# Kernel optimization log

Measured on AMD Instinct MI355X. Metric: run time of the kernel, lower is better.

The kernel has to match this reference:

```python
import jax, jax.numpy as jnp
import numpy as np

# dims
N, T, F, DEMO, H, NHEAD, K, GCN, FFN = 4096, 48, 76, 4, 252, 4, 10, 256, 128
D = H + DEMO          # 256, input dim to graph constructor / clustering / gcn
DK = D // NHEAD       # 64
TAU, MASK_P, LAMBDA_KL, LAMBDA_CL, PHI_INIT, ALPHA = 0.5, 0.1, 1.0, 1.0, 3.0 / N, 1.0


def setup_inputs() -> dict:
    key = jax.random.key(0)
    ks = jax.random.split(key, 16)
    s = 0.02
    return dict(
        x=jax.random.normal(ks[0], (N, T, F), jnp.float32),
        x_demo=jax.random.normal(ks[1], (N, DEMO), jnp.float32),
        sorted_length=jax.random.randint(ks[2], (N,), 1, T + 1),
        mask_edge=jax.random.uniform(ks[3], (N, N), jnp.float32),
        w_ih=jax.random.normal(ks[4], (3 * H, F), jnp.float32) * s,
        w_hh=jax.random.normal(ks[5], (3 * H, H), jnp.float32) * s,
        b_ih=jnp.zeros((3 * H,), jnp.float32),
        b_hh=jnp.zeros((3 * H,), jnp.float32),
        h0=jnp.zeros((H,), jnp.float32),
        wq=jax.random.normal(ks[6], (D, D), jnp.float32) * s,
        bq=jnp.zeros((D,), jnp.float32),
        wk=jax.random.normal(ks[7], (D, D), jnp.float32) * s,
        bk=jnp.zeros((D,), jnp.float32),
        wo=jax.random.normal(ks[8], (NHEAD,), jnp.float32) * s,
        bo=jnp.zeros((), jnp.float32),
        phi=jnp.float32(PHI_INIT),
        centers=jax.random.normal(ks[9], (K, D), jnp.float32),
        gcn_w=jax.random.normal(ks[10], (D, GCN), jnp.float32) * s,
        gcn_b=jnp.zeros((GCN,), jnp.float32),
        ffn_w=jax.random.normal(ks[11], (GCN, FFN), jnp.float32) * s,
        ffn_b=jnp.zeros((FFN,), jnp.float32),
        pre_w=jax.random.normal(ks[12], (GCN, 2), jnp.float32) * s,
        pre_b=jnp.zeros((2,), jnp.float32),
    )


def _forward(x, x_demo, sorted_length, mask_edge, w_ih, w_hh, b_ih, b_hh, h0,
             wq, bq, wk, bk, wo, bo, phi, centers, gcn_w, gcn_b,
             ffn_w, ffn_b, pre_w, pre_b):
    n = x.shape[0]

    # --- GRU over time (torch nn.GRU equations), scan over T ---
    def gru_step(h, xt):
        gi = xt @ w_ih.T + b_ih                     # [N, 3H]
        gh = h @ w_hh.T + b_hh
        ir, iz, inn = jnp.split(gi, 3, axis=-1)
        hr, hz, hn = jnp.split(gh, 3, axis=-1)
        r = jax.nn.sigmoid(ir + hr)
        zg = jax.nn.sigmoid(iz + hz)
        ng = jnp.tanh(inn + r * hn)
        h = (1.0 - zg) * ng + zg * h
        return h, h

    _, outs = jax.lax.scan(gru_step, jnp.broadcast_to(h0, (n, H)), jnp.swapaxes(x, 0, 1))
    idx = jnp.clip(sorted_length - 1, 0, T - 1)
    x_gru = outs[idx, jnp.arange(n)]                # last valid hidden state [N, H]
    x_star = jnp.concatenate([x_gru, x_demo], axis=1)  # [N, D]

    # --- GraphConstructor: multi-head attention adjacency ---
    q = (x_star @ wq.T + bq).reshape(n, NHEAD, DK)
    kk = (x_star @ wk.T + bk).reshape(n, NHEAD, DK)
    scores = jnp.einsum('nhd,mhd->nmh', q, kk) / np.sqrt(DK)  # [N, N, h]
    scores = scores @ wo + bo                                  # Wo: Linear(h, 1)
    attn = jax.nn.softmax(scores, axis=1)
    eye = jnp.eye(n, dtype=x.dtype)
    adj = jnp.where(attn >= phi, 1.0, 0.0) * (1.0 - eye)       # threshold, zero diag

    # --- Clustering: soft assignment around given centers (KMeans fit replaced
    #     by fixed cluster_layer parameter; same soft-assign / KLD math) ---
    d2 = jnp.sum((x_star[:, None, :] - centers[None]) ** 2, axis=-1)  # [N, K]
    qsoft = 1.0 / (1.0 + d2 / ALPHA)
    qsoft = qsoft / jnp.sum(qsoft, axis=1, keepdims=True)
    pdist = qsoft ** 2 / jnp.sum(qsoft, axis=0, keepdims=True)
    pdist = jax.lax.stop_gradient(pdist / jnp.sum(pdist, axis=1, keepdims=True))
    label = jnp.argmax(qsoft, axis=1)
    kl_loss = jnp.mean(jnp.sum(pdist * jnp.log(pdist / (qsoft + 1e-6)), axis=-1))

    # --- GCNConv on dense adjacency (sym-normalized with self loops) ---
    xw = x_star @ gcn_w

    def gcn(a):
        a_hat = a + eye
        dinv = 1.0 / jnp.sqrt(jnp.sum(a_hat, axis=1))
        return (dinv[:, None] * a_hat * dinv[None, :]) @ xw + gcn_b

    z = gcn(adj)
    adj_aug = adj * (mask_edge >= MASK_P).astype(x.dtype)  # DataAug edge mask (bernoulli keep 1-p)
    z_aug = gcn(adj_aug)
    zf = z @ ffn_w + ffn_b
    zfa = z_aug @ ffn_w + ffn_b

    # --- clloss: NxN contrastive loss ---
    def l2n(a):
        return a / jnp.clip(jnp.linalg.norm(a, axis=1, keepdims=True), 1e-12, None)

    zn, zan = l2n(zf), l2n(zfa)
    intra = jnp.exp(zn @ zn.T / TAU)
    inter = jnp.exp(zn @ zan.T / TAU)
    cadj = (label[:, None] == label[None, :]).astype(x.dtype) * (1.0 - eye)
    cadj_new = jnp.where(adj == 1.0, 0.0, cadj)
    positive = jnp.diag(inter) + jnp.sum(intra * adj, axis=1) + jnp.sum(intra * cadj_new, axis=1)
    denom = jnp.sum(intra, axis=1) + jnp.sum(inter, axis=1) - jnp.diag(intra)
    cnt = jnp.sum(adj, axis=1) + jnp.sum(cadj_new, axis=1) + 1.0
    cl_loss = -jnp.sum(jnp.log(positive / denom) / cnt)

    loss = LAMBDA_KL * kl_loss + LAMBDA_CL * cl_loss
    output = z @ pre_w + pre_b
    return output, loss


def reference(x, x_demo, sorted_length, mask_edge, w_ih, w_hh, b_ih, b_hh, h0,
              wq, bq, wk, bk, wo, bo, phi, centers, gcn_w, gcn_b,
              ffn_w, ffn_b, pre_w, pre_b):
    return _forward(x, x_demo, sorted_length, mask_edge, w_ih, w_hh, b_ih, b_hh, h0,
                    wq, bq, wk, bk, wo, bo, phi, centers, gcn_w, gcn_b,
                    ffn_w, ffn_b, pre_w, pre_b)
```

## Files before the change

kernel.cpp:

```cpp
#include <hip/hip_runtime.h>
#include <cstdint>
#include <cstddef>

typedef _Float16 f16;
typedef f16 f16x8 __attribute__((ext_vector_type(8)));
typedef float f32x4 __attribute__((ext_vector_type(4)));

#define MFMA(a,b,c) __builtin_amdgcn_mfma_f32_16x16x32_f16(a,b,c,0,0,0)

__device__ __forceinline__ float sigm(float x){ return 1.f/(1.f+__expf(-x)); }
__device__ __forceinline__ float tanh_f(float x){
  float a = __expf(-2.f*fabsf(x));
  float t = (1.f-a)/(1.f+a);
  return x >= 0.f ? t : -t;
}
__device__ __forceinline__ uint16_t f2bf(float f){
  uint32_t u = __float_as_uint(f);
  return (uint16_t)((u + 0x7fffu + ((u>>16)&1u)) >> 16);
}
__device__ __forceinline__ float bf2f(uint16_t h){
  return __uint_as_float(((uint32_t)h) << 16);
}

__global__ __launch_bounds__(256) void k_prep(
    const float* __restrict__ w_ih, const float* __restrict__ w_hh,
    const float* __restrict__ b_ih, const float* __restrict__ b_hh,
    const int* __restrict__ slen,
    const float* __restrict__ wq, const float* __restrict__ wk,
    const float* __restrict__ gcn_w,
    f16* __restrict__ BgT, f16* __restrict__ wq16, f16* __restrict__ wk16,
    f16* __restrict__ gw16, float* __restrict__ biasc, int* __restrict__ idx)
{
  int id = blockIdx.x*256 + threadIdx.x;
  if (id < 360448){
    int g = id / (256*352); int rem = id % (256*352);
    int j = rem / 352; int k = rem % 352;
    float v = 0.f;
    if (j < 252){
      if (k < 96){
        if (k < 76 && g != 3){
          int row = (g==2) ? (504+j) : (g*252+j);
          v = w_ih[row*76 + k];
        }
      } else {
        int kh = k - 96;
        if (kh < 252 && g != 2){
          int row = (g==3) ? (504+j) : (g*252+j);
          v = w_hh[row*252 + kh];
        }
      }
    }
    BgT[id] = (f16)v;
    return;
  }
  id -= 360448;
  if (id < 65536){ wq16[id] = (f16)wq[id]; return; }
  id -= 65536;
  if (id < 65536){ wk16[id] = (f16)wk[id]; return; }
  id -= 65536;
  if (id < 65536){ int j = id >> 8, d = id & 255; gw16[id] = (f16)gcn_w[d*256 + j]; return; }
  id -= 65536;
  if (id < 1008){
    int g = id / 252, j = id % 252; float v;
    if (g==0) v = b_ih[j] + b_hh[j];
    else if (g==1) v = b_ih[252+j] + b_hh[252+j];
    else if (g==2) v = b_ih[504+j];
    else v = b_hh[504+j];
    biasc[id] = v; return;
  }
  id -= 1008;
  if (id < 4096){
    int s = slen[id] - 1; s = s < 0 ? 0 : (s > 47 ? 47 : s);
    idx[id] = s; return;
  }
}

__global__ __launch_bounds__(256) void k_xt(const float* __restrict__ x,
    f16* __restrict__ x16t)
{
  int id = blockIdx.x*256 + threadIdx.x;
  int c = id % 12; int rem = id / 12;
  int n = rem & 4095; int t = rem >> 12;
  const float* xp = x + ((size_t)n*48 + t)*76;
  f16x8 o;
  #pragma unroll
  for (int e = 0; e < 8; ++e){
    int k = c*8 + e;
    o[e] = (k < 76) ? (f16)xp[k] : (f16)0.f;
  }
  *(f16x8*)(x16t + ((size_t)t*4096 + n)*96 + c*8) = o;
}

__global__ __launch_bounds__(1024, 4) void k_gru_all(
    const f16* __restrict__ x16t, const f16* __restrict__ BgT,
    const float* __restrict__ biasc, const float* __restrict__ h0,
    const int* __restrict__ idxp, float* __restrict__ xstar,
    f16* __restrict__ xs16)
{
  __shared__ f16 hbuf[2][32][256];
  __shared__ f16 wc[7][16][512];
  __shared__ int idxl[32];
  int lane = threadIdx.x & 63, w = threadIdx.x >> 6;
  int l16 = lane & 15, lq = lane >> 4;
  int nb = blockIdx.x * 32;

  for (int i = threadIdx.x; i < 32*256; i += 1024){
    int row = i >> 8, c = i & 255;
    int sc = (((c >> 3) ^ (row & 7)) << 3) | (c & 7);
    hbuf[0][row][sc] = (c < 252) ? (f16)h0[c] : (f16)0.f;
  }
  if (threadIdx.x < 32) idxl[threadIdx.x] = idxp[nb + threadIdx.x];

  int j = w*16 + l16;
  bool jv = (j < 252);
  int js = jv ? j : 251;
  float bR = biasc[js], bZ = biasc[252+js], bI = biasc[504+js], bH = biasc[756+js];
  const f16* pR = BgT + (size_t)(0*256 + j)*352 + lq*8;
  const f16* pZ = BgT + (size_t)(1*256 + j)*352 + lq*8;
  const f16* pI = BgT + (size_t)(2*256 + j)*352 + lq*8;
  const f16* pH = BgT + (size_t)(3*256 + j)*352 + lq*8;
  const f16* xp0 = x16t + ((size_t)nb + l16)*96 + lq*8;
  const f16* xp1 = x16t + ((size_t)nb + 16 + l16)*96 + lq*8;

  *(f16x8*)&wc[0][w][lane*8] = *(const f16x8*)(pR);
  *(f16x8*)&wc[1][w][lane*8] = *(const f16x8*)(pZ);
  *(f16x8*)&wc[2][w][lane*8] = *(const f16x8*)(pI);
  *(f16x8*)&wc[3][w][lane*8] = *(const f16x8*)(pR + 32);
  *(f16x8*)&wc[4][w][lane*8] = *(const f16x8*)(pZ + 32);
  *(f16x8*)&wc[5][w][lane*8] = *(const f16x8*)(pI + 32);
  *(f16x8*)&wc[6][w][lane*8] = *(const f16x8*)(pR + 64);

  float hown[2][4];
  #pragma unroll
  for (int mf = 0; mf < 2; ++mf)
  #pragma unroll
  for (int r = 0; r < 4; ++r)
    hown[mf][r] = jv ? h0[js] : 0.f;

  __syncthreads();

  for (int t = 0; t < 48; ++t){
    const f16 (*hin)[256] = hbuf[t & 1];
    f16 (*hout)[256]      = hbuf[(t & 1) ^ 1];
    f32x4 z4 = {0.f,0.f,0.f,0.f};
    f32x4 aR[2] = {z4,z4}, aZ[2] = {z4,z4}, aI[2] = {z4,z4}, aH[2] = {z4,z4};
    size_t xt = (size_t)t*4096*96;

    f16x8 R0,Z0,M0, R1,Z1,M1, R2,Z2,M2, R3,Z3,M3;
#define PIN3(s) asm volatile("" :: "v"(*(const f32x4*)&R##s), \
                                   "v"(*(const f32x4*)&Z##s), \
                                   "v"(*(const f32x4*)&M##s))
#define PIN2(s) asm volatile("" :: "v"(*(const f32x4*)&Z##s), \
                                   "v"(*(const f32x4*)&M##s))
#define LW(s,u) do{ \
      R##s = *(const f16x8*)(pR + (u)*32); \
      Z##s = *(const f16x8*)(pZ + (u)*32); \
      M##s = *(const f16x8*)((((u) < 3) ? pI : pH) + (u)*32); \
      PIN3(s); }while(0)
#define LW2(s,u) do{ \
      Z##s = *(const f16x8*)(pZ + (u)*32); \
      M##s = *(const f16x8*)((((u) < 3) ? pI : pH) + (u)*32); \
      PIN2(s); }while(0)
#define MM(u, wR_, wZ_, wM_, a0, a1) do{ \
      aR[0] = MFMA(a0, wR_, aR[0]);  aR[1] = MFMA(a1, wR_, aR[1]); \
      aZ[0] = MFMA(a0, wZ_, aZ[0]);  aZ[1] = MFMA(a1, wZ_, aZ[1]); \
      if ((u) < 3){ aI[0] = MFMA(a0, wM_, aI[0]);  aI[1] = MFMA(a1, wM_, aI[1]); } \
      else        { aH[0] = MFMA(a0, wM_, aH[0]);  aH[1] = MFMA(a1, wM_, aH[1]); } \
    }while(0)
#define STEP(s,u) do{ \
      f16x8 a0, a1; \
      if ((u) < 3){ \
        a0 = *(const f16x8*)(xp0 + xt + (u)*32); \
        a1 = *(const f16x8*)(xp1 + xt + (u)*32); \
      } else { \
        int chunk = ((u) - 3)*4 + lq; \
        a0 = *(const f16x8*)(&hin[l16][(chunk ^ (l16 & 7)) << 3]); \
        a1 = *(const f16x8*)(&hin[16 + l16][(chunk ^ (l16 & 7)) << 3]); \
      } \
      MM(u, R##s, Z##s, M##s, a0, a1); \
    }while(0)
#define STEP_L(u) do{ \
      f16x8 wR_ = *(const f16x8*)&wc[(u)*3+0][w][lane*8]; \
      f16x8 wZ_ = *(const f16x8*)&wc[(u)*3+1][w][lane*8]; \
      f16x8 wM_ = *(const f16x8*)&wc[(u)*3+2][w][lane*8]; \
      f16x8 a0 = *(const f16x8*)(xp0 + xt + (u)*32); \
      f16x8 a1 = *(const f16x8*)(xp1 + xt + (u)*32); \
      MM(u, wR_, wZ_, wM_, a0, a1); \
    }while(0)
#define STEP2(s,u) do{ \
      f16x8 wR_ = *(const f16x8*)&wc[6][w][lane*8]; \
      f16x8 a0 = *(const f16x8*)(xp0 + xt + (u)*32); \
      f16x8 a1 = *(const f16x8*)(xp1 + xt + (u)*32); \
      MM(u, wR_, Z##s, M##s, a0, a1); \
    }while(0)

    LW2(0,2); LW(1,3); LW(2,4); LW(3,5);
    STEP_L(0);
    STEP_L(1);
    STEP2(0,2);  LW(0,6);
    STEP(1,3);   LW(1,7);
    STEP(2,4);   LW(2,8);
    STEP(3,5);   LW(3,9);
    STEP(0,6);   LW(0,10);
    STEP(1,7);
    STEP(2,8);
    STEP(3,9);
    STEP(0,10);
#undef LW
#undef LW2
#undef STEP
#undef STEP_L
#undef STEP2
#undef MM
#undef PIN3
#undef PIN2

    #pragma unroll
    for (int mf = 0; mf < 2; ++mf)
    #pragma unroll
    for (int r = 0; r < 4; ++r){
      int row = mf*16 + lq*4 + r;
      float rr = sigm(aR[mf][r] + bR);
      float zz = sigm(aZ[mf][r] + bZ);
      float ng = tanh_f(aI[mf][r] + bI + rr*(aH[mf][r] + bH));
      float hnew = (1.f - zz)*ng + zz*hown[mf][r];
      hnew = jv ? hnew : 0.f;
      hown[mf][r] = hnew;
      int sc = (((j >> 3) ^ (row & 7)) << 3) | (j & 7);
      hout[row][sc] = (f16)hnew;
      if (jv && idxl[row] == t){
        xstar[((size_t)(nb + row) << 8) + j] = hnew;
        xs16[((size_t)(nb + row) << 8) + j] = (f16)hnew;
      }
    }
    __syncthreads();
  }
}

__global__ __launch_bounds__(256) void k_xdemo(const float* __restrict__ x_demo,
    float* __restrict__ xs32, f16* __restrict__ xs16)
{
  int id = blockIdx.x*256 + threadIdx.x;
  int n = id >> 2, c = id & 3;
  float v = x_demo[id];
  xs32[((size_t)n << 8) + 252 + c] = v;
  xs16[((size_t)n << 8) + 252 + c] = (f16)v;
}

template<int MODE>
__global__ __launch_bounds__(256) void k_proj(const f16* __restrict__ xs16,
    const f16* __restrict__ w16, const float* __restrict__ bias,
    const float* __restrict__ wo, f16* __restrict__ out16)
{
  int lane = threadIdx.x & 63, wv = threadIdx.x >> 6;
  int l16 = lane & 15, lq = lane >> 4;
  int nb = blockIdx.x * 64;
  int ocol = blockIdx.y*64 + wv*16 + l16;
  f32x4 z4 = {0.f,0.f,0.f,0.f};
  f32x4 acc[4] = {z4,z4,z4,z4};
  #pragma unroll
  for (int ks = 0; ks < 8; ++ks){
    f16x8 b = *(const f16x8*)(w16 + (size_t)ocol*256 + ks*32 + lq*8);
    #pragma unroll
    for (int mi = 0; mi < 4; ++mi){
      f16x8 a = *(const f16x8*)(xs16 + (size_t)(nb + mi*16 + l16)*256 + ks*32 + lq*8);
      acc[mi] = MFMA(a, b, acc[mi]);
    }
  }
  float badd = bias[ocol];
  float scale = (MODE == 0) ? wo[ocol >> 6]*0.125f : 1.f;
  #pragma unroll
  for (int mi = 0; mi < 4; ++mi)
  #pragma unroll
  for (int r = 0; r < 4; ++r){
    int n = nb + mi*16 + lq*4 + r;
    float v = acc[mi][r] + badd;
    if (MODE == 0) v *= scale;
    out16[(size_t)n*256 + ocol] = (f16)v;
  }
}

__global__ __launch_bounds__(256) void k_scores(const f16* __restrict__ qf,
    const f16* __restrict__ kf, uint16_t* __restrict__ sco)
{
  int lane = threadIdx.x & 63, w = threadIdx.x >> 6;
  int l16 = lane & 15, lq = lane >> 4;
  int mh = w >> 1, jh = w & 1;
  int nb = blockIdx.x*128 + mh*64;
  int mb = blockIdx.y*128 + jh*64;
  f32x4 z4 = {0.f,0.f,0.f,0.f};
  f32x4 acc[4][4];
  #pragma unroll
  for (int i = 0; i < 4; ++i)
  #pragma unroll
  for (int j = 0; j < 4; ++j) acc[i][j] = z4;
  #pragma unroll
  for (int ks = 0; ks < 8; ++ks){
    f16x8 a[4], b[4];
    #pragma unroll
    for (int i = 0; i < 4; ++i){
      a[i] = *(const f16x8*)(qf + (size_t)(nb + i*16 + l16)*256 + ks*32 + lq*8);
      b[i] = *(const f16x8*)(kf + (size_t)(mb + i*16 + l16)*256 + ks*32 + lq*8);
    }
    #pragma unroll
    for (int mi = 0; mi < 4; ++mi)
    #pragma unroll
    for (int jf = 0; jf < 4; ++jf)
      acc[mi][jf] = MFMA(a[mi], b[jf], acc[mi][jf]);
  }
  #pragma unroll
  for (int mi = 0; mi < 4; ++mi)
  #pragma unroll
  for (int jf = 0; jf < 4; ++jf)
  #pragma unroll
  for (int r = 0; r < 4; ++r){
    int n = nb + mi*16 + lq*4 + r;
    int m = mb + jf*16 + l16;
    sco[((size_t)n << 12) + m] = f2bf(acc[mi][jf][r]);
  }
}

__global__ __launch_bounds__(256) void k_adj(const uint16_t* __restrict__ sco,
    const float* __restrict__ mask_edge, const float* __restrict__ phip,
    uint8_t* __restrict__ flags, float* __restrict__ sadj,
    float* __restrict__ dinv, float* __restrict__ dinva)
{
  int n = blockIdx.x;
  int lane = threadIdx.x & 63, wv = threadIdx.x >> 6;
  const uint16_t* row = sco + ((size_t)n << 12);
  int base = threadIdx.x * 16;
  const uint4* p = (const uint4*)(row + base);
  uint4 w0 = p[0], w1 = p[1];
  uint32_t ws_[8] = {w0.x,w0.y,w0.z,w0.w,w1.x,w1.y,w1.z,w1.w};
  float v[16];
  #pragma unroll
  for (int i = 0; i < 8; ++i){
    v[2*i]   = bf2f((uint16_t)(ws_[i] & 0xffffu));
    v[2*i+1] = bf2f((uint16_t)(ws_[i] >> 16));
  }
  float mx = v[0];
  #pragma unroll
  for (int i = 1; i < 16; ++i) mx = fmaxf(mx, v[i]);
  #pragma unroll
  for (int o = 32; o >= 1; o >>= 1) mx = fmaxf(mx, __shfl_xor(mx, o));
  __shared__ float redA[4], redB[4], redC[4], redD[4];
  if (lane == 0) redA[wv] = mx;
  __syncthreads();
  mx = fmaxf(fmaxf(redA[0], redA[1]), fmaxf(redA[2], redA[3]));
  float s = 0.f;
  #pragma unroll
  for (int i = 0; i < 16; ++i){ v[i] = __expf(v[i] - mx); s += v[i]; }
  #pragma unroll
  for (int o = 32; o >= 1; o >>= 1) s += __shfl_xor(s, o);
  if (lane == 0) redB[wv] = s;
  __syncthreads();
  float rs = 1.f / (redB[0] + redB[1] + redB[2] + redB[3]);
  float phi = phip[0];
  uint32_t by[16]; int c0 = 0, c1 = 0;
  #pragma unroll
  for (int e = 0; e < 16; ++e){
    float a = v[e] * rs;
    int col = base + e;
    uint32_t b = (a >= phi && col != n) ? 1u : 0u;
    if (b){ if (mask_edge[((size_t)n << 12) + col] >= 0.1f) b |= 2u; }
    by[e] = b;
    c0 += (int)(b & 1u);
    c1 += (int)(b >> 1);
  }
  uint4 pk;
  pk.x = by[0]  | (by[1]  << 8) | (by[2]  << 16) | (by[3]  << 24);
  pk.y = by[4]  | (by[5]  << 8) | (by[6]  << 16) | (by[7]  << 24);
  pk.z = by[8]  | (by[9]  << 8) | (by[10] << 16) | (by[11] << 24);
  pk.w = by[12] | (by[13] << 8) | (by[14] << 16) | (by[15] << 24);
  *(uint4*)(flags + ((size_t)n << 12) + base) = pk;
  float f0 = (float)c0, f1 = (float)c1;
  #pragma unroll
  for (int o = 32; o >= 1; o >>= 1){ f0 += __shfl_xor(f0, o); f1 += __shfl_xor(f1, o); }
  if (lane == 0){ redC[wv] = f0; redD[wv] = f1; }
  __syncthreads();
  if (threadIdx.x == 0){
    float d0 = redC[0]+redC[1]+redC[2]+redC[3];
    float d1 = redD[0]+redD[1]+redD[2]+redD[3];
    sadj[n] = d0;
    dinv[n]  = rsqrtf(1.f + d0);
    dinva[n] = rsqrtf(1.f + d1);
  }
}

__global__ __launch_bounds__(256) void k_xw_y(const f16* __restrict__ xs16,
    const f16* __restrict__ gw16, const float* __restrict__ dinv,
    const float* __restrict__ dinva, f16* __restrict__ y16, f16* __restrict__ ya16)
{
  int lane = threadIdx.x & 63, wv = threadIdx.x >> 6;
  int l16 = lane & 15, lq = lane >> 4;
  int nb = blockIdx.x * 64;
  int jcol = blockIdx.y*64 + wv*16 + l16;
  f32x4 z4 = {0.f,0.f,0.f,0.f};
  f32x4 acc[4] = {z4,z4,z4,z4};
  #pragma unroll
  for (int ks = 0; ks < 8; ++ks){
    f16x8 b = *(const f16x8*)(gw16 + (size_t)jcol*256 + ks*32 + lq*8);
    #pragma unroll
    for (int mi = 0; mi < 4; ++mi){
      f16x8 a = *(const f16x8*)(xs16 + (size_t)(nb + mi*16 + l16)*256 + ks*32 + lq*8);
      acc[mi] = MFMA(a, b, acc[mi]);
    }
  }
  #pragma unroll
  for (int mi = 0; mi < 4; ++mi)
  #pragma unroll
  for (int r = 0; r < 4; ++r){
    int n = nb + mi*16 + lq*4 + r;
    float v = acc[mi][r];
    y16[(size_t)n*256 + jcol]  = (f16)(dinv[n]*v);
    ya16[(size_t)n*256 + jcol] = (f16)(dinva[n]*v);
  }
}

__global__ __launch_bounds__(256) void k_zgather(const uint8_t* __restrict__ flags,
    const f16* __restrict__ y16, const f16* __restrict__ ya16,
    const float* __restrict__ dinv, const float* __restrict__ dinva,
    const float* __restrict__ gcn_b, float* __restrict__ z32, float* __restrict__ za32)
{
  int n = blockIdx.x;
  int lane = threadIdx.x & 63, wv = threadIdx.x >> 6;
  uint4 w = ((const uint4*)(flags + ((size_t)n << 12)))[threadIdx.x];
  uint32_t m0[4] = {w.x & 0x01010101u, w.y & 0x01010101u, w.z & 0x01010101u, w.w & 0x01010101u};
  uint32_t m1[4] = {w.x & 0x02020202u, w.y & 0x02020202u, w.z & 0x02020202u, w.w & 0x02020202u};
  int c0 = __popc(m0[0]) + __popc(m0[1]) + __popc(m0[2]) + __popc(m0[3]);
  int c1 = __popc(m1[0]) + __popc(m1[1]) + __popc(m1[2]) + __popc(m1[3]);
  int v0 = c0, v1 = c1;
  #pragma unroll
  for (int o = 1; o < 64; o <<= 1){
    int u0 = __shfl_up(v0, o), u1 = __shfl_up(v1, o);
    if (lane >= o){ v0 += u0; v1 += u1; }
  }
  __shared__ int wsum0[4], wsum1[4];
  if (lane == 63){ wsum0[wv] = v0; wsum1[wv] = v1; }
  __syncthreads();
  int pos0 = v0 - c0, pos1 = v1 - c1;
  #pragma unroll
  for (int i = 0; i < 4; ++i) if (i < wv){ pos0 += wsum0[i]; pos1 += wsum1[i]; }
  int tot0 = wsum0[0]+wsum0[1]+wsum0[2]+wsum0[3];
  int tot1 = wsum1[0]+wsum1[1]+wsum1[2]+wsum1[3];
  __shared__ uint16_t list0[4096];
  __shared__ uint16_t list1[4096];
  int cbase = threadIdx.x * 16;
  #pragma unroll
  for (int q = 0; q < 4; ++q){
    uint32_t m = m0[q];
    while (m){
      int b = __ffs(m) - 1;
      list0[pos0++] = (uint16_t)(cbase + q*4 + (b >> 3));
      m &= m - 1;
    }
    m = m1[q];
    while (m){
      int b = __ffs(m) - 1;
      list1[pos1++] = (uint16_t)(cbase + q*4 + (b >> 3));
      m &= m - 1;
    }
  }
  __syncthreads();
  int j = threadIdx.x;
  float acc0 = (float)y16[((size_t)n << 8) + j];
  float acc1 = (float)ya16[((size_t)n << 8) + j];
  for (int i = 0; i < tot0; ++i) acc0 += (float)y16[((size_t)list0[i] << 8) + j];
  for (int i = 0; i < tot1; ++i) acc1 += (float)ya16[((size_t)list1[i] << 8) + j];
  z32[((size_t)n << 8) + j]  = dinv[n]*acc0 + gcn_b[j];
  za32[((size_t)n << 8) + j] = dinva[n]*acc1 + gcn_b[j];
}

__global__ __launch_bounds__(256) void k_cluster(const float* __restrict__ xs32,
    const float* __restrict__ centers, float* __restrict__ qsoft,
    int* __restrict__ labels, float* __restrict__ colsum)
{
  int nb = blockIdx.x * 16;
  __shared__ float xs[16][256];
  __shared__ float ct[2560];
  __shared__ float d2s[16][10];
  __shared__ float qs[16][10];
  for (int i = threadIdx.x; i < 16*256; i += 256) xs[i >> 8][i & 255] = xs32[(size_t)nb*256 + i];
  for (int i = threadIdx.x; i < 2560; i += 256){ int k = i >> 8, d = i & 255; ct[d*10 + k] = centers[i]; }
  __syncthreads();
  if (threadIdx.x < 160){
    int r = threadIdx.x / 10, k = threadIdx.x % 10;
    float s = 0.f;
    for (int d = 0; d < 256; ++d){ float df = xs[r][d] - ct[d*10 + k]; s += df*df; }
    d2s[r][k] = s;
  }
  __syncthreads();
  if (threadIdx.x < 16){
    int r = threadIdx.x;
    float un[10]; float tot = 0.f;
    #pragma unroll
    for (int k = 0; k < 10; ++k){ un[k] = 1.f/(1.f + d2s[r][k]); tot += un[k]; }
    float inv = 1.f / tot;
    int best = 0; float bm = un[0];
    #pragma unroll
    for (int k = 1; k < 10; ++k){ if (un[k] > bm){ bm = un[k]; best = k; } }
    labels[nb + r] = best;
    #pragma unroll
    for (int k = 0; k < 10; ++k){ float q = un[k]*inv; qs[r][k] = q; qsoft[(size_t)(nb + r)*10 + k] = q; }
  }
  __syncthreads();
  if (threadIdx.x < 10){
    int k = threadIdx.x; float s = 0.f;
    #pragma unroll
    for (int r = 0; r < 16; ++r) s += qs[r][k];
    atomicAdd(&colsum[k], s);
  }
}

__global__ __launch_bounds__(256) void k_kl(const float* __restrict__ qsoft,
    const float* __restrict__ colsum, float* __restrict__ klsum)
{
  int n = blockIdx.x*256 + threadIdx.x;
  float p[10]; float s = 0.f;
  #pragma unroll
  for (int k = 0; k < 10; ++k){
    float q = qsoft[(size_t)n*10 + k];
    float pu = q*q/colsum[k];
    p[k] = pu; s += pu;
  }
  float inv = 1.f/s; float kl = 0.f;
  #pragma unroll
  for (int k = 0; k < 10; ++k){
    float pk = p[k]*inv;
    float q = qsoft[(size_t)n*10 + k];
    kl += pk*__logf(pk/(q + 1e-6f));
  }
  int lane = threadIdx.x & 63, wv = threadIdx.x >> 6;
  #pragma unroll
  for (int o = 32; o >= 1; o >>= 1) kl += __shfl_xor(kl, o);
  __shared__ float red[4];
  if (lane == 0) red[wv] = kl;
  __syncthreads();
  if (threadIdx.x == 0) atomicAdd(klsum, red[0]+red[1]+red[2]+red[3]);
}

__global__ __launch_bounds__(128) void k_ffn(const float* __restrict__ z32,
    const float* __restrict__ za32, const float* __restrict__ ffn_w,
    const float* __restrict__ ffn_b, f16* __restrict__ zn16, f16* __restrict__ zan16)
{
  int n = blockIdx.x; int aug = blockIdx.y;
  const float* z = (aug ? za32 : z32) + ((size_t)n << 8);
  __shared__ float zr[256];
  zr[threadIdx.x] = z[threadIdx.x];
  zr[threadIdx.x + 128] = z[threadIdx.x + 128];
  __syncthreads();
  int j = threadIdx.x;
  float acc = ffn_b[j];
  #pragma unroll 8
  for (int d = 0; d < 256; ++d) acc += zr[d]*ffn_w[d*128 + j];
  float ss = acc*acc;
  int lane = threadIdx.x & 63, wv = threadIdx.x >> 6;
  #pragma unroll
  for (int o = 32; o >= 1; o >>= 1) ss += __shfl_xor(ss, o);
  __shared__ float sred[2];
  if (lane == 0) sred[wv] = ss;
  __syncthreads();
  float tot = sred[0] + sred[1];
  float rn = 1.f / fmaxf(sqrtf(tot), 1e-12f);
  (aug ? zan16 : zn16)[((size_t)n << 7) + j] = (f16)(acc*rn);
}

__global__ __launch_bounds__(256) void k_closs(const f16* __restrict__ zn,
    const f16* __restrict__ zan, const uint8_t* __restrict__ flags,
    const int* __restrict__ labels,
    float* __restrict__ rs1, float* __restrict__ rs2, float* __restrict__ rsA,
    float* __restrict__ rsC, float* __restrict__ rcC, float* __restrict__ rdI,
    float* __restrict__ rdi)
{
  int lane = threadIdx.x & 63;
  int ji = threadIdx.x >> 6;
  int l16 = lane & 15, lq = lane >> 4;
  int nb = blockIdx.x * 32;
  int mstart = blockIdx.y * 512;
  f16x8 A[2][4];
  #pragma unroll
  for (int mi = 0; mi < 2; ++mi)
  #pragma unroll
  for (int ks = 0; ks < 4; ++ks)
    A[mi][ks] = *(const f16x8*)(zn + (size_t)(nb + mi*16 + l16)*128 + ks*32 + lq*8);
  int labn[8];
  #pragma unroll
  for (int i = 0; i < 8; ++i) labn[i] = labels[nb + (i >> 2)*16 + lq*4 + (i & 3)];
  float a1[8]={}, a2[8]={}, aA[8]={}, aC[8]={}, aCc[8]={}, adI[8]={}, adi[8]={};
  uint8_t fA[8]; int labA;
  {
    int mcol0 = mstart + ji*16 + l16;
    #pragma unroll
    for (int i = 0; i < 8; ++i){
      int n = nb + (i >> 2)*16 + lq*4 + (i & 3);
      fA[i] = flags[((size_t)n << 12) + mcol0];
    }
    labA = labels[mcol0];
  }
  #pragma unroll
  for (int tile = 0; tile < 8; ++tile){
    int mcol = mstart + tile*64 + ji*16 + l16;
    uint8_t fB[8]; int labB = 0;
    if (tile < 7){
      int mn = mcol + 64;
      #pragma unroll
      for (int i = 0; i < 8; ++i){
        int n = nb + (i >> 2)*16 + lq*4 + (i & 3);
        fB[i] = flags[((size_t)n << 12) + mn];
      }
      labB = labels[mn];
    }
    f32x4 z4 = {0.f,0.f,0.f,0.f};
    f32x4 acc1[2] = {z4, z4};
    f32x4 acc2[2] = {z4, z4};
    #pragma unroll
    for (int ks = 0; ks < 4; ++ks){
      f16x8 b1 = *(const f16x8*)(zn  + (size_t)mcol*128 + ks*32 + lq*8);
      f16x8 b2 = *(const f16x8*)(zan + (size_t)mcol*128 + ks*32 + lq*8);
      #pragma unroll
      for (int mi = 0; mi < 2; ++mi){
        acc1[mi] = MFMA(A[mi][ks], b1, acc1[mi]);
        acc2[mi] = MFMA(A[mi][ks], b2, acc2[mi]);
      }
    }
    #pragma unroll
    for (int mi = 0; mi < 2; ++mi)
    #pragma unroll
    for (int r = 0; r < 4; ++r){
      int i8 = mi*4 + r;
      int n = nb + mi*16 + lq*4 + r;
      float e1 = __expf(2.f*acc1[mi][r]);
      float e2 = __expf(2.f*acc2[mi][r]);
      uint8_t fl = fA[i8];
      a1[i8] += e1; a2[i8] += e2;
      bool adjb = (fl & 1);
      if (adjb) aA[i8] += e1;
      if (!adjb && labn[i8] == labA && n != mcol){ aC[i8] += e1; aCc[i8] += 1.f; }
      if (n == mcol){ adI[i8] += e2; adi[i8] += e1; }
    }
    if (tile < 7){
      #pragma unroll
      for (int i = 0; i < 8; ++i) fA[i] = fB[i];
      labA = labB;
    }
  }
  #pragma unroll
  for (int i = 0; i < 8; ++i){
    #pragma unroll
    for (int o = 1; o < 16; o <<= 1){
      a1[i]  += __shfl_xor(a1[i], o);  a2[i]  += __shfl_xor(a2[i], o);
      aA[i]  += __shfl_xor(aA[i], o);  aC[i]  += __shfl_xor(aC[i], o);
      aCc[i] += __shfl_xor(aCc[i], o); adI[i] += __shfl_xor(adI[i], o);
      adi[i] += __shfl_xor(adi[i], o);
    }
  }
  if (l16 == 0){
    #pragma unroll
    for (int i = 0; i < 8; ++i){
      int n = nb + (i >> 2)*16 + lq*4 + (i & 3);
      atomicAdd(&rs1[n], a1[i]);  atomicAdd(&rs2[n], a2[i]);
      atomicAdd(&rsA[n], aA[i]);  atomicAdd(&rsC[n], aC[i]);
      atomicAdd(&rcC[n], aCc[i]); atomicAdd(&rdI[n], adI[i]);
      atomicAdd(&rdi[n], adi[i]);
    }
  }
}

__global__ __launch_bounds__(256) void k_clfinal(const float* __restrict__ rs1,
    const float* __restrict__ rs2, const float* __restrict__ rsA,
    const float* __restrict__ rsC, const float* __restrict__ rcC,
    const float* __restrict__ rdI, const float* __restrict__ rdi,
    const float* __restrict__ sadj, float* __restrict__ clsum)
{
  int n = blockIdx.x*256 + threadIdx.x;
  float pos = rdI[n] + rsA[n] + rsC[n];
  float den = rs1[n] + rs2[n] - rdi[n];
  float cnt = sadj[n] + rcC[n] + 1.f;
  float v = __logf(pos/den)/cnt;
  int lane = threadIdx.x & 63, wv = threadIdx.x >> 6;
  #pragma unroll
  for (int o = 32; o >= 1; o >>= 1) v += __shfl_xor(v, o);
  __shared__ float red[4];
  if (lane == 0) red[wv] = v;
  __syncthreads();
  if (threadIdx.x == 0) atomicAdd(clsum, red[0]+red[1]+red[2]+red[3]);
}

__global__ void k_loss(const float* __restrict__ scal, float* __restrict__ out){
  out[8192] = scal[0]*(1.f/4096.f) - scal[1];
}

__global__ __launch_bounds__(256) void k_outhead(const float* __restrict__ z32,
    const float* __restrict__ pre_w, const float* __restrict__ pre_b,
    float* __restrict__ out)
{
  int lane = threadIdx.x & 63, wv = threadIdx.x >> 6;
  int n = blockIdx.x*4 + wv;
  float4 zv = *(const float4*)(z32 + ((size_t)n << 8) + lane*4);
  float4 w0 = *(const float4*)(pre_w + lane*8);
  float4 w1 = *(const float4*)(pre_w + lane*8 + 4);
  float c0 = zv.x*w0.x + zv.y*w0.z + zv.z*w1.x + zv.w*w1.z;
  float c1 = zv.x*w0.y + zv.y*w0.w + zv.z*w1.y + zv.w*w1.w;
  #pragma unroll
  for (int o = 32; o >= 1; o >>= 1){ c0 += __shfl_xor(c0, o); c1 += __shfl_xor(c1, o); }
  if (lane == 0){
    out[(size_t)n*2]     = c0 + pre_b[0];
    out[(size_t)n*2 + 1] = c1 + pre_b[1];
  }
}

extern "C" void kernel_launch(void* const* d_in, const int* in_sizes, int n_in,
                              void* d_out, int out_size, void* d_ws, size_t ws_size,
                              hipStream_t stream)
{
  const float* x         = (const float*)d_in[0];
  const float* x_demo    = (const float*)d_in[1];
  const int*   slen      = (const int*)d_in[2];
  const float* mask_edge = (const float*)d_in[3];
  const float* w_ih      = (const float*)d_in[4];
  const float* w_hh      = (const float*)d_in[5];
  const float* b_ih      = (const float*)d_in[6];
  const float* b_hh      = (const float*)d_in[7];
  const float* h0        = (const float*)d_in[8];
  const float* wq        = (const float*)d_in[9];
  const float* bq        = (const float*)d_in[10];
  const float* wk        = (const float*)d_in[11];
  const float* bk        = (const float*)d_in[12];
  const float* wo        = (const float*)d_in[13];
  const float* phi       = (const float*)d_in[15];
  const float* centers   = (const float*)d_in[16];
  const float* gcn_w     = (const float*)d_in[17];
  const float* gcn_b     = (const float*)d_in[18];
  const float* ffn_w     = (const float*)d_in[19];
  const float* ffn_b     = (const float*)d_in[20];
  const float* pre_w     = (const float*)d_in[21];
  const float* pre_b     = (const float*)d_in[22];
  float* out = (float*)d_out;

  size_t off = 0;
  char* base = (char*)d_ws;
  auto take = [&](size_t bytes)->void*{
    void* p = base + off;
    off += (bytes + 255) & ~(size_t)255;
    return p;
  };
  f16*   BgT    = (f16*)take((size_t)4*256*352*2);
  f16*   wq16   = (f16*)take((size_t)65536*2);
  f16*   wk16   = (f16*)take((size_t)65536*2);
  f16*   gw16   = (f16*)take((size_t)65536*2);
  float* biasc  = (float*)take(1008*4);
  int*   idx    = (int*)take(4096*4);
  float* xs32   = (float*)take((size_t)4096*256*4);
  f16*   xs16   = (f16*)take((size_t)4096*256*2);
  f16*   qf16   = (f16*)take((size_t)4096*256*2);
  f16*   kf16   = (f16*)take((size_t)4096*256*2);
  uint16_t* sco = (uint16_t*)take((size_t)4096*4096*2);
  uint8_t* flags= (uint8_t*)take((size_t)4096*4096);
  float* sadj   = (float*)take(4096*4);
  float* dinv   = (float*)take(4096*4);
  float* dinva  = (float*)take(4096*4);
  f16*   y16    = (f16*)take((size_t)4096*256*2);
  f16*   ya16   = (f16*)take((size_t)4096*256*2);
  float* z32    = (float*)take((size_t)4096*256*4);
  float* za32   = (float*)take((size_t)4096*256*4);
  f16*   zn16   = (f16*)take((size_t)4096*128*2);
  f16*   zan16  = (f16*)take((size_t)4096*128*2);
  float* qsoft  = (float*)take((size_t)4096*10*4);
  int*   labels = (int*)take(4096*4);
  float* colsum = (float*)take(64);
  float* scal   = (float*)take(64);
  float* rsbuf  = (float*)take((size_t)7*4096*4);
  float* rs1 = rsbuf,        *rs2 = rsbuf + 4096, *rsA = rsbuf + 2*4096;
  float* rsC = rsbuf + 3*4096, *rcC = rsbuf + 4*4096;
  float* rdI = rsbuf + 5*4096, *rdi = rsbuf + 6*4096;

  f16* x16t = (f16*)sco;

  hipMemsetAsync(colsum, 0, 64, stream);
  hipMemsetAsync(scal, 0, 64, stream);
  hipMemsetAsync(rsbuf, 0, (size_t)7*4096*4, stream);

  k_prep<<<2196, 256, 0, stream>>>(w_ih, w_hh, b_ih, b_hh, slen, wq, wk, gcn_w,
                                   BgT, wq16, wk16, gw16, biasc, idx);
  k_xt<<<9216, 256, 0, stream>>>(x, x16t);
  k_xdemo<<<64, 256, 0, stream>>>(x_demo, xs32, xs16);
  k_gru_all<<<128, 1024, 0, stream>>>(x16t, BgT, biasc, h0, idx, xs32, xs16);
  k_proj<0><<<dim3(64, 4), 256, 0, stream>>>(xs16, wq16, bq, wo, qf16);
  k_proj<1><<<dim3(64, 4), 256, 0, stream>>>(xs16, wk16, bk, wo, kf16);
  k_scores<<<dim3(32, 32), 256, 0, stream>>>(qf16, kf16, sco);
  k_adj<<<4096, 256, 0, stream>>>(sco, mask_edge, phi, flags, sadj, dinv, dinva);
  k_xw_y<<<dim3(64, 4), 256, 0, stream>>>(xs16, gw16, dinv, dinva, y16, ya16);
  k_zgather<<<4096, 256, 0, stream>>>(flags, y16, ya16, dinv, dinva, gcn_b, z32, za32);
  k_cluster<<<256, 256, 0, stream>>>(xs32, centers, qsoft, labels, colsum);
  k_kl<<<16, 256, 0, stream>>>(qsoft, colsum, &scal[0]);
  k_ffn<<<dim3(4096, 2), 128, 0, stream>>>(z32, za32, ffn_w, ffn_b, zn16, zan16);
  k_closs<<<dim3(128, 8), 256, 0, stream>>>(zn16, zan16, flags, labels,
                                            rs1, rs2, rsA, rsC, rcC, rdI, rdi);
  k_clfinal<<<16, 256, 0, stream>>>(rs1, rs2, rsA, rsC, rcC, rdI, rdi, sadj, &scal[1]);
  k_loss<<<1, 1, 0, stream>>>(scal, out);
  k_outhead<<<1024, 256, 0, stream>>>(z32, pre_w, pre_b, out);

  (void)in_sizes; (void)n_in; (void)out_size; (void)ws_size;
}
```

Measured before the change: 801.0 us.

## Single-buffer GRU hidden state, cache more weights in LDS, merge Q/K projections

The GRU kernel drops the double-buffered hidden-state array for one buffer with an extra barrier per step. It caches one more weight fragment (Z for the third chunk) in LDS, keeps the per-row output indices in registers instead of shared memory, and uses nontemporal loads for the streamed weights. The two Q/K projection launches become one kernel with a doubled grid. The extra barrier adds per-step sync cost in the serial recurrence, while the LDS and register savings and the dropped launch reduce overhead.

```diff
diff --git a/kernel.cpp b/kernel.cpp
--- a/kernel.cpp
+++ b/kernel.cpp
@@ -97,9 +97,8 @@
     const int* __restrict__ idxp, float* __restrict__ xstar,
     f16* __restrict__ xs16)
 {
-  __shared__ f16 hbuf[2][32][256];
-  __shared__ f16 wc[7][16][512];
-  __shared__ int idxl[32];
+  __shared__ f16 hbuf[32][256];
+  __shared__ f16 wc[8][16][512];
   int lane = threadIdx.x & 63, w = threadIdx.x >> 6;
   int l16 = lane & 15, lq = lane >> 4;
   int nb = blockIdx.x * 32;
@@ -107,9 +106,8 @@
   for (int i = threadIdx.x; i < 32*256; i += 1024){
     int row = i >> 8, c = i & 255;
     int sc = (((c >> 3) ^ (row & 7)) << 3) | (c & 7);
-    hbuf[0][row][sc] = (c < 252) ? (f16)h0[c] : (f16)0.f;
-  }
-  if (threadIdx.x < 32) idxl[threadIdx.x] = idxp[nb + threadIdx.x];
+    hbuf[row][sc] = (c < 252) ? (f16)h0[c] : (f16)0.f;
+  }
 
   int j = w*16 + l16;
   bool jv = (j < 252);
@@ -129,19 +127,23 @@
   *(f16x8*)&wc[4][w][lane*8] = *(const f16x8*)(pZ + 32);
   *(f16x8*)&wc[5][w][lane*8] = *(const f16x8*)(pI + 32);
   *(f16x8*)&wc[6][w][lane*8] = *(const f16x8*)(pR + 64);
+  *(f16x8*)&wc[7][w][lane*8] = *(const f16x8*)(pZ + 64);
 
   float hown[2][4];
+  int idxr[2][4];
   #pragma unroll
   for (int mf = 0; mf < 2; ++mf)
   #pragma unroll
-  for (int r = 0; r < 4; ++r)
+  for (int r = 0; r < 4; ++r){
     hown[mf][r] = jv ? h0[js] : 0.f;
-
-  __syncthreads();
+    idxr[mf][r] = idxp[nb + mf*16 + lq*4 + r];
+  }
+
+  __syncthreads();
+
+#define NTL(p) __builtin_nontemporal_load((const f16x8*)(p))
 
   for (int t = 0; t < 48; ++t){
-    const f16 (*hin)[256] = hbuf[t & 1];
-    f16 (*hout)[256]      = hbuf[(t & 1) ^ 1];
     f32x4 z4 = {0.f,0.f,0.f,0.f};
     f32x4 aR[2] = {z4,z4}, aZ[2] = {z4,z4}, aI[2] = {z4,z4}, aH[2] = {z4,z4};
     size_t xt = (size_t)t*4096*96;
@@ -150,17 +152,15 @@
 #define PIN3(s) asm volatile("" :: "v"(*(const f32x4*)&R##s), \
                                    "v"(*(const f32x4*)&Z##s), \
                                    "v"(*(const f32x4*)&M##s))
-#define PIN2(s) asm volatile("" :: "v"(*(const f32x4*)&Z##s), \
-                                   "v"(*(const f32x4*)&M##s))
+#define PIN1(s) asm volatile("" :: "v"(*(const f32x4*)&M##s))
 #define LW(s,u) do{ \
-      R##s = *(const f16x8*)(pR + (u)*32); \
-      Z##s = *(const f16x8*)(pZ + (u)*32); \
-      M##s = *(const f16x8*)((((u) < 3) ? pI : pH) + (u)*32); \
+      R##s = NTL(pR + (u)*32); \
+      Z##s = NTL(pZ + (u)*32); \
+      M##s = NTL(pH + (u)*32); \
       PIN3(s); }while(0)
-#define LW2(s,u) do{ \
-      Z##s = *(const f16x8*)(pZ + (u)*32); \
-      M##s = *(const f16x8*)((((u) < 3) ? pI : pH) + (u)*32); \
-      PIN2(s); }while(0)
+#define LW1(s) do{ \
+      M##s = NTL(pI + 64); \
+      PIN1(s); }while(0)
 #define MM(u, wR_, wZ_, wM_, a0, a1) do{ \
       aR[0] = MFMA(a0, wR_, aR[0]);  aR[1] = MFMA(a1, wR_, aR[1]); \
       aZ[0] = MFMA(a0, wZ_, aZ[0]);  aZ[1] = MFMA(a1, wZ_, aZ[1]); \
@@ -168,15 +168,9 @@
       else        { aH[0] = MFMA(a0, wM_, aH[0]);  aH[1] = MFMA(a1, wM_, aH[1]); } \
     }while(0)
 #define STEP(s,u) do{ \
-      f16x8 a0, a1; \
-      if ((u) < 3){ \
-        a0 = *(const f16x8*)(xp0 + xt + (u)*32); \
-        a1 = *(const f16x8*)(xp1 + xt + (u)*32); \
-      } else { \
-        int chunk = ((u) - 3)*4 + lq; \
-        a0 = *(const f16x8*)(&hin[l16][(chunk ^ (l16 & 7)) << 3]); \
-        a1 = *(const f16x8*)(&hin[16 + l16][(chunk ^ (l16 & 7)) << 3]); \
-      } \
+      int chunk = ((u) - 3)*4 + lq; \
+      f16x8 a0 = *(const f16x8*)(&hbuf[l16][(chunk ^ (l16 & 7)) << 3]); \
+      f16x8 a1 = *(const f16x8*)(&hbuf[16 + l16][(chunk ^ (l16 & 7)) << 3]); \
       MM(u, R##s, Z##s, M##s, a0, a1); \
     }while(0)
 #define STEP_L(u) do{ \
@@ -187,17 +181,18 @@
       f16x8 a1 = *(const f16x8*)(xp1 + xt + (u)*32); \
       MM(u, wR_, wZ_, wM_, a0, a1); \
     }while(0)
-#define STEP2(s,u) do{ \
+#define STEP2(s) do{ \
       f16x8 wR_ = *(const f16x8*)&wc[6][w][lane*8]; \
-      f16x8 a0 = *(const f16x8*)(xp0 + xt + (u)*32); \
-      f16x8 a1 = *(const f16x8*)(xp1 + xt + (u)*32); \
-      MM(u, wR_, Z##s, M##s, a0, a1); \
+      f16x8 wZ_ = *(const f16x8*)&wc[7][w][lane*8]; \
+      f16x8 a0 = *(const f16x8*)(xp0 + xt + 64); \
+      f16x8 a1 = *(const f16x8*)(xp1 + xt + 64); \
+      MM(2, wR_, wZ_, M##s, a0, a1); \
     }while(0)
 
-    LW2(0,2); LW(1,3); LW(2,4); LW(3,5);
+    LW1(0); LW(1,3); LW(2,4); LW(3,5);
     STEP_L(0);
     STEP_L(1);
-    STEP2(0,2);  LW(0,6);
+    STEP2(0);    LW(0,6);
     STEP(1,3);   LW(1,7);
     STEP(2,4);   LW(2,8);
     STEP(3,5);   LW(3,9);
@@ -207,13 +202,15 @@
     STEP(3,9);
     STEP(0,10);
 #undef LW
-#undef LW2
+#undef LW1
 #undef STEP
 #undef STEP_L
 #undef STEP2
 #undef MM
 #undef PIN3
-#undef PIN2
+#undef PIN1
+
+    __syncthreads();
 
     #pragma unroll
     for (int mf = 0; mf < 2; ++mf)
@@ -227,14 +224,15 @@
       hnew = jv ? hnew : 0.f;
       hown[mf][r] = hnew;
       int sc = (((j >> 3) ^ (row & 7)) << 3) | (j & 7);
-      hout[row][sc] = (f16)hnew;
-      if (jv && idxl[row] == t){
+      hbuf[row][sc] = (f16)hnew;
+      if (jv && idxr[mf][r] == t){
         xstar[((size_t)(nb + row) << 8) + j] = hnew;
         xs16[((size_t)(nb + row) << 8) + j] = (f16)hnew;
       }
     }
     __syncthreads();
   }
+#undef NTL
 }
 
 __global__ __launch_bounds__(256) void k_xdemo(const float* __restrict__ x_demo,
@@ -247,15 +245,20 @@
   xs16[((size_t)n << 8) + 252 + c] = (f16)v;
 }
 
-template<int MODE>
-__global__ __launch_bounds__(256) void k_proj(const f16* __restrict__ xs16,
-    const f16* __restrict__ w16, const float* __restrict__ bias,
-    const float* __restrict__ wo, f16* __restrict__ out16)
+__global__ __launch_bounds__(256) void k_projqk(const f16* __restrict__ xs16,
+    const f16* __restrict__ wq16, const f16* __restrict__ wk16,
+    const float* __restrict__ bq, const float* __restrict__ bk,
+    const float* __restrict__ wo, f16* __restrict__ qf, f16* __restrict__ kf)
 {
   int lane = threadIdx.x & 63, wv = threadIdx.x >> 6;
   int l16 = lane & 15, lq = lane >> 4;
   int nb = blockIdx.x * 64;
-  int ocol = blockIdx.y*64 + wv*16 + l16;
+  int mode = blockIdx.y >> 2;
+  int yy = blockIdx.y & 3;
+  const f16* w16 = mode ? wk16 : wq16;
+  const float* bias = mode ? bk : bq;
+  f16* out16 = mode ? kf : qf;
+  int ocol = yy*64 + wv*16 + l16;
   f32x4 z4 = {0.f,0.f,0.f,0.f};
   f32x4 acc[4] = {z4,z4,z4,z4};
   #pragma unroll
@@ -268,14 +271,14 @@
     }
   }
   float badd = bias[ocol];
-  float scale = (MODE == 0) ? wo[ocol >> 6]*0.125f : 1.f;
+  float scale = mode ? 1.f : wo[ocol >> 6]*0.125f;
   #pragma unroll
   for (int mi = 0; mi < 4; ++mi)
   #pragma unroll
   for (int r = 0; r < 4; ++r){
     int n = nb + mi*16 + lq*4 + r;
     float v = acc[mi][r] + badd;
-    if (MODE == 0) v *= scale;
+    if (!mode) v *= scale;
     out16[(size_t)n*256 + ocol] = (f16)v;
   }
 }
@@ -785,8 +788,7 @@
   k_xt<<<9216, 256, 0, stream>>>(x, x16t);
   k_xdemo<<<64, 256, 0, stream>>>(x_demo, xs32, xs16);
   k_gru_all<<<128, 1024, 0, stream>>>(x16t, BgT, biasc, h0, idx, xs32, xs16);
-  k_proj<0><<<dim3(64, 4), 256, 0, stream>>>(xs16, wq16, bq, wo, qf16);
-  k_proj<1><<<dim3(64, 4), 256, 0, stream>>>(xs16, wk16, bk, wo, kf16);
+  k_projqk<<<dim3(64, 8), 256, 0, stream>>>(xs16, wq16, wk16, bq, bk, wo, qf16, kf16);
   k_scores<<<dim3(32, 32), 256, 0, stream>>>(qf16, kf16, sco);
   k_adj<<<4096, 256, 0, stream>>>(sco, mask_edge, phi, flags, sadj, dinv, dinva);
   k_xw_y<<<dim3(64, 4), 256, 0, stream>>>(xs16, gw16, dinv, dinva, y16, ya16);
```

New measurement: 1.108 ms. 1.38x slower.
